# Performance work log

Measured on AMD Instinct MI355X. Metric: run time of the kernel, lower is better.

## Reference

```python
import jax, jax.numpy as jnp
import numpy as np

S_DIM, H_DIM, A_DIM, EMB, MAX_LEN = 1024, 2048, 166, 256, 20
DEC = H_DIM // 2          # decoder_hidden = 1024
VOCAB = A_DIM + 3         # 169; sos=166, eos=167, pad/ignore=168
SOS, IGNORE = A_DIM, A_DIM + 2
B = 8192


def setup_inputs() -> dict:
    key = jax.random.key(0)
    ks = jax.random.split(key, 12)
    sc = lambda fan: 1.0 / np.sqrt(fan)
    emb = jax.random.normal(ks[0], (VOCAB, EMB), jnp.float32)
    emb = emb.at[IGNORE].set(0.0)  # padding_idx=168 row is zero
    return {
        's': jax.random.normal(ks[1], (B, S_DIM), jnp.float32),
        'a_target_seq': jax.random.randint(ks[2], (B, MAX_LEN), 0, VOCAB, jnp.int32),
        'W1': jax.random.normal(ks[3], (S_DIM, H_DIM), jnp.float32) * sc(S_DIM),
        'b1': jnp.zeros((H_DIM,), jnp.float32),
        'W2': jax.random.normal(ks[4], (H_DIM, DEC), jnp.float32) * sc(H_DIM),
        'b2': jnp.zeros((DEC,), jnp.float32),
        'emb': emb,
        'Wih': jax.random.normal(ks[5], (EMB + DEC, 3 * DEC), jnp.float32) * sc(DEC),
        'Whh': jax.random.normal(ks[6], (DEC, 3 * DEC), jnp.float32) * sc(DEC),
        'bih': jnp.zeros((3 * DEC,), jnp.float32),
        'bhh': jnp.zeros((3 * DEC,), jnp.float32),
        'Wp': jax.random.normal(ks[7], (DEC, VOCAB), jnp.float32) * sc(DEC),
        'bp': jnp.zeros((VOCAB,), jnp.float32),
    }


def _gru_step(h, x, Wih, Whh, bih, bhh):
    # torch nn.GRU cell: gates ordered (r, z, n)
    gi = x @ Wih + bih                      # [B, 3H]
    gh = h @ Whh + bhh                      # [B, 3H]
    ir, iz, inn = jnp.split(gi, 3, axis=-1)
    hr, hz, hn = jnp.split(gh, 3, axis=-1)
    r = jax.nn.sigmoid(ir + hr)
    z = jax.nn.sigmoid(iz + hz)
    n = jnp.tanh(inn + r * hn)
    return (1.0 - z) * n + z * h


def reference(s, a_target_seq, W1, b1, W2, b2, emb, Wih, Whh, bih, bhh, Wp, bp):
    b = s.shape[0]
    h_s = jax.nn.relu(s @ W1 + b1) @ W2 + b2      # net(s): [B, DEC]
    h0 = h_s                                      # concatenated at every step
    # teacher forcing: input token at step t is SOS for t=0 else a_target_seq[:, t-1]
    toks = jnp.concatenate([jnp.full((b, 1), SOS, a_target_seq.dtype),
                            a_target_seq[:, :-1]], axis=1)      # [B, T]

    def step(h, tok_t):
        x = jnp.concatenate([emb[tok_t], h0], axis=-1)          # [B, EMB+DEC]
        h_new = _gru_step(h, x, Wih, Whh, bih, bhh)
        logits = h_new @ Wp + bp                                # [B, VOCAB]
        return h_new, logits

    _, logits_seq = jax.lax.scan(step, h_s, toks.T)             # [T, B, V]
    logits = jnp.transpose(logits_seq, (1, 0, 2))               # [B, T, V]

    # CrossEntropyLoss(ignore_index=IGNORE), mean over non-ignored targets
    flat_logits = logits.reshape(-1, VOCAB)
    flat_tgt = a_target_seq.reshape(-1)
    logp = jax.nn.log_softmax(flat_logits, axis=-1)
    nll = -jnp.take_along_axis(logp, flat_tgt[:, None].astype(jnp.int32), axis=-1)[:, 0]
    mask = (flat_tgt != IGNORE).astype(nll.dtype)
    loss_pred = jnp.sum(nll * mask) / jnp.maximum(jnp.sum(mask), 1.0)

    # pred_act_tsr: scatter 1.0 at per-step argmax, then drop last 3 special tokens
    eval_a = jnp.argmax(logits, axis=-1)                        # [B, T]
    pred_act_tsr = jnp.zeros((b, VOCAB), logits.dtype)
    pred_act_tsr = pred_act_tsr.at[jnp.arange(b)[:, None], eval_a].set(1.0)
    return loss_pred, pred_act_tsr[:, :-3]
```

## Files before the change

kernel.cpp:

```cpp
#include <hip/hip_runtime.h>
#include <math.h>

typedef _Float16 f16;
typedef _Float16 half8 __attribute__((ext_vector_type(8)));
typedef _Float16 half4v __attribute__((ext_vector_type(4)));
typedef float f32x4 __attribute__((ext_vector_type(4)));

#define BATCH 8192
#define SDIM  1024
#define HDIM  2048
#define DECD  1024
#define EMBD  256
#define G3    3072
#define VOCAB 169
#define VPAD  176
#define NFRAG 11
#define TLEN  20
#define SOS_TOK 166
#define IGN_TOK 168
#define OUTC  166

#define GLOAD16(gp, lp) __builtin_amdgcn_global_load_lds( \
    (const __attribute__((address_space(1))) unsigned int*)(gp), \
    (__attribute__((address_space(3))) unsigned int*)(lp), 16, 0, 0)

__device__ __forceinline__ void split2(float a, f16& h, f16& l)
{
    float hi = (fabsf(a) >= 6.103515625e-05f) ? (float)(f16)a : 0.0f;
    h = (f16)hi;
    l = (f16)((a - hi) * 2048.0f);
}

__device__ __forceinline__ float join2(f16 h, f16 l)
{
    return (float)h + (float)l * 4.8828125e-4f;
}

__device__ __forceinline__ int swz(int r, int k0)
{
    const int line = r >> 1;
    const int s = (((r & 1) << 2) | (k0 >> 3)) ^ (line & 7);
    return line * 64 + s * 8;
}

template<int MODE>
__global__ __launch_bounds__(256, 2)
void gemm16(const f16* __restrict__ Ah, const f16* __restrict__ Al,
            const f16* __restrict__ Bh, const f16* __restrict__ Bl,
            const float* __restrict__ bias, float* __restrict__ C,
            f16* __restrict__ Ch, f16* __restrict__ Cl,
            int M, int N, int K, int relu)
{
    __shared__ __align__(16) f16 lds[4][4096];

    const int nx = N >> 7;
    const int cpx = gridDim.x >> 3;
    int wg = blockIdx.x;
    wg = (wg & 7) * cpx + (wg >> 3);
    const int m0 = (wg / nx) << 7;
    const int n0 = (wg % nx) << 7;

    const int tid = threadIdx.x;
    const int w = tid >> 6;
    const int lane = tid & 63;
    const int wr = w >> 1, wc = w & 1;

    const int qq = (lane & 7) ^ (lane >> 3);
    const int row_off = ((lane >> 3) << 1) | (qq >> 2);
    const int k_off = (qq & 3) << 3;
    const f16* sb = (w == 0) ? Ah + (size_t)m0 * K
                  : (w == 1) ? Al + (size_t)m0 * K
                  : (w == 2) ? Bh + (size_t)n0 * K
                             : Bl + (size_t)n0 * K;
    sb += (size_t)row_off * K + k_off;
    f16* lb = &lds[w][0];

    int offA[4], offB[4];
    {
        const int fr = lane & 15, k0 = (lane >> 4) << 3;
#pragma unroll
        for (int t = 0; t < 4; ++t) {
            offA[t] = swz(wr * 64 + t * 16 + fr, k0);
            offB[t] = swz(wc * 64 + t * 16 + fr, k0);
        }
    }

    f32x4 acch[4][4], accl[4][4];
#pragma unroll
    for (int i = 0; i < 4; ++i)
#pragma unroll
        for (int j = 0; j < 4; ++j) { acch[i][j] = (f32x4)0.0f; accl[i][j] = (f32x4)0.0f; }

    const int nkt = K >> 5;
    const size_t K16 = (size_t)K * 16;
    for (int kt = 0; kt < nkt; ++kt) {
        const f16* s = sb + kt * 32;
#pragma unroll
        for (int i = 0; i < 8; ++i)
            GLOAD16(s + (size_t)i * K16, lb + i * 512);
        __syncthreads();

        half8 fah[4], fbh[4], fal[4], fbl[4];
#pragma unroll
        for (int t = 0; t < 4; ++t) {
            fah[t] = *(const half8*)&lds[0][offA[t]];
            fal[t] = *(const half8*)&lds[1][offA[t]];
            fbh[t] = *(const half8*)&lds[2][offB[t]];
            fbl[t] = *(const half8*)&lds[3][offB[t]];
        }
#pragma unroll
        for (int i = 0; i < 4; ++i)
#pragma unroll
            for (int j = 0; j < 4; ++j) {
                acch[i][j] = __builtin_amdgcn_mfma_f32_16x16x32_f16(fah[i], fbh[j], acch[i][j], 0, 0, 0);
                accl[i][j] = __builtin_amdgcn_mfma_f32_16x16x32_f16(fal[i], fbh[j], accl[i][j], 0, 0, 0);
                accl[i][j] = __builtin_amdgcn_mfma_f32_16x16x32_f16(fah[i], fbl[j], accl[i][j], 0, 0, 0);
            }
        __syncthreads();
    }

    const float inv2048 = 4.8828125e-4f;
    const int fr = lane & 15;
    const int fq = lane >> 4;
#pragma unroll
    for (int j = 0; j < 4; ++j) {
        const int col = n0 + wc * 64 + j * 16 + fr;
        const float bc = bias[col];
#pragma unroll
        for (int i = 0; i < 4; ++i) {
            const int row0 = m0 + wr * 64 + i * 16 + fq * 4;
            const f32x4 vh = acch[i][j], vl = accl[i][j];
#pragma unroll
            for (int r = 0; r < 4; ++r) {
                float v = vh[r] + vl[r] * inv2048 + bc;
                if (relu) v = fmaxf(v, 0.0f);
                const size_t o = (size_t)(row0 + r) * N + col;
                if constexpr (MODE & 1) C[o] = v;
                if constexpr (MODE & 2) { f16 hh, hl; split2(v, hh, hl); Ch[o] = hh; Cl[o] = hl; }
            }
        }
    }
}

#define STAGE(SET, KT) do {                                                        \
    const int ko_ = (KT) * 32 + k_off;                                             \
    if (w == 0) {                                                                  \
        const f16* sp = hch + (size_t)(m0 + row_off) * DECD + ko_;                 \
        _Pragma("unroll") for (int i_ = 0; i_ < 8; ++i_)                           \
            GLOAD16(sp + (size_t)i_ * (16 * DECD), &lds[SET][i_ * 512]);           \
    } else if (w == 1) {                                                           \
        const f16* sp = hcl + (size_t)(m0 + row_off) * DECD + ko_;                 \
        _Pragma("unroll") for (int i_ = 0; i_ < 8; ++i_)                           \
            GLOAD16(sp + (size_t)i_ * (16 * DECD), &lds[SET][4096 + i_ * 512]);    \
    } else if (w == 2) {                                                           \
        _Pragma("unroll") for (int g_ = 0; g_ < 3; ++g_) {                         \
            const f16* sp = whh + (size_t)(g_ * DECD + n0 + row_off) * DECD + ko_; \
            _Pragma("unroll") for (int i_ = 0; i_ < 4; ++i_)                       \
                GLOAD16(sp + (size_t)i_ * (16 * DECD),                             \
                        &lds[SET][8192 + g_ * 4096 + i_ * 512]);                   \
        }                                                                          \
    } else {                                                                       \
        _Pragma("unroll") for (int g_ = 0; g_ < 3; ++g_) {                         \
            const f16* sp = whl + (size_t)(g_ * DECD + n0 + row_off) * DECD + ko_; \
            _Pragma("unroll") for (int i_ = 0; i_ < 4; ++i_)                       \
                GLOAD16(sp + (size_t)i_ * (16 * DECD),                             \
                        &lds[SET][8192 + g_ * 4096 + 2048 + i_ * 512]);            \
        }                                                                          \
    }                                                                              \
} while (0)

__global__ __launch_bounds__(256, 1)
void gru_fused(const f16* __restrict__ hch, const f16* __restrict__ hcl,
               const f16* __restrict__ whh, const f16* __restrict__ whl,
               const float* __restrict__ bhh, const float* __restrict__ gx0,
               const float* __restrict__ tg, const int* __restrict__ tseq,
               int t, f16* __restrict__ hnh, f16* __restrict__ hnl)
{
    __shared__ __align__(16) f16 lds[2][20480];

    const int cpx = gridDim.x >> 3;
    int wg = blockIdx.x;
    wg = (wg & 7) * cpx + (wg >> 3);
    const int m0 = (wg >> 4) << 7;
    const int n0 = (wg & 15) << 6;

    const int tid = threadIdx.x, w = tid >> 6, lane = tid & 63;
    const int wr = w >> 1, wc = w & 1;

    const int qq = (lane & 7) ^ (lane >> 3);
    const int row_off = ((lane >> 3) << 1) | (qq >> 2);
    const int k_off = (qq & 3) << 3;

    const int fr = lane & 15, kq8 = (lane >> 4) << 3;
    int offA[4], offB[2];
#pragma unroll
    for (int i = 0; i < 4; ++i) offA[i] = swz(wr * 64 + i * 16 + fr, kq8);
#pragma unroll
    for (int j = 0; j < 2; ++j) offB[j] = swz(wc * 32 + j * 16 + fr, kq8);

    f32x4 aH[3][4][2], aL[3][4][2];
#pragma unroll
    for (int g = 0; g < 3; ++g)
#pragma unroll
        for (int i = 0; i < 4; ++i)
#pragma unroll
            for (int j = 0; j < 2; ++j) { aH[g][i][j] = (f32x4)0.0f; aL[g][i][j] = (f32x4)0.0f; }

    STAGE(0, 0);
    __syncthreads();

#pragma unroll 2
    for (int kt = 0; kt < DECD / 32; ++kt) {
        const int cur = kt & 1;
        if (kt < DECD / 32 - 1) STAGE(cur ^ 1, kt + 1);

        half8 fah[4], fal[4];
#pragma unroll
        for (int i = 0; i < 4; ++i) {
            fah[i] = *(const half8*)&lds[cur][offA[i]];
            fal[i] = *(const half8*)&lds[cur][4096 + offA[i]];
        }
#pragma unroll
        for (int g = 0; g < 3; ++g) {
            half8 bh[2], bl[2];
#pragma unroll
            for (int j = 0; j < 2; ++j) {
                bh[j] = *(const half8*)&lds[cur][8192 + g * 4096 + offB[j]];
                bl[j] = *(const half8*)&lds[cur][8192 + g * 4096 + 2048 + offB[j]];
            }
#pragma unroll
            for (int i = 0; i < 4; ++i)
#pragma unroll
                for (int j = 0; j < 2; ++j) {
                    aH[g][i][j] = __builtin_amdgcn_mfma_f32_16x16x32_f16(fah[i], bh[j], aH[g][i][j], 0, 0, 0);
                    aL[g][i][j] = __builtin_amdgcn_mfma_f32_16x16x32_f16(fal[i], bh[j], aL[g][i][j], 0, 0, 0);
                    aL[g][i][j] = __builtin_amdgcn_mfma_f32_16x16x32_f16(fah[i], bl[j], aL[g][i][j], 0, 0, 0);
                }
        }
        __syncthreads();
    }

    const float inv = 4.8828125e-4f;
    const int fq = lane >> 4;
    float br[2], bz[2], bn[2];
#pragma unroll
    for (int j = 0; j < 2; ++j) {
        const int col = n0 + wc * 32 + j * 16 + fr;
        br[j] = bhh[col];
        bz[j] = bhh[DECD + col];
        bn[j] = bhh[2 * DECD + col];
    }
#pragma unroll
    for (int i = 0; i < 4; ++i) {
#pragma unroll
        for (int r = 0; r < 4; ++r) {
            const int row = m0 + wr * 64 + i * 16 + fq * 4 + r;
            const int tok = (t == 0) ? SOS_TOK : tseq[(size_t)row * TLEN + (t - 1)];
            const size_t gb = (size_t)row * G3;
            const size_t tb = (size_t)tok * G3;
#pragma unroll
            for (int j = 0; j < 2; ++j) {
                const int col = n0 + wc * 32 + j * 16 + fr;
                const float ghr = aH[0][i][j][r] + aL[0][i][j][r] * inv + br[j];
                const float ghz = aH[1][i][j][r] + aL[1][i][j][r] * inv + bz[j];
                const float ghn = aH[2][i][j][r] + aL[2][i][j][r] * inv + bn[j];
                const float gir = gx0[gb + col] + tg[tb + col];
                const float giz = gx0[gb + DECD + col] + tg[tb + DECD + col];
                const float gin = gx0[gb + 2 * DECD + col] + tg[tb + 2 * DECD + col];
                const float rr = 1.f / (1.f + expf(-(gir + ghr)));
                const float zz = 1.f / (1.f + expf(-(giz + ghz)));
                const float nn = tanhf(gin + rr * ghn);
                const size_t hidx = (size_t)row * DECD + col;
                const float hp = join2(hch[hidx], hcl[hidx]);
                const float hv = (1.f - zz) * nn + zz * hp;
                f16 a_, b_; split2(hv, a_, b_);
                hnh[hidx] = a_;
                hnl[hidx] = b_;
            }
        }
    }
}

__global__ __launch_bounds__(256)
void transpose_split(const float* __restrict__ Wm, f16* __restrict__ th, f16* __restrict__ tl,
                     int K, int N)
{
    __shared__ float tile[32][33];
    const int n0 = blockIdx.x << 5, k0 = blockIdx.y << 5;
    const int tx = threadIdx.x & 31, ty = threadIdx.x >> 5;
#pragma unroll
    for (int j = 0; j < 32; j += 8)
        tile[ty + j][tx] = Wm[(size_t)(k0 + ty + j) * N + n0 + tx];
    __syncthreads();
#pragma unroll
    for (int j = 0; j < 32; j += 8) {
        const float a = tile[tx][ty + j];
        f16 hh, hl; split2(a, hh, hl);
        const size_t o = (size_t)(n0 + ty + j) * K + k0 + tx;
        th[o] = hh; tl[o] = hl;
    }
}

__global__ __launch_bounds__(256)
void wp_split(const float* __restrict__ Wp, f16* __restrict__ wph, f16* __restrict__ wpl)
{
    const int k = blockIdx.x * 256 + threadIdx.x;
    const int n = blockIdx.y;
    const float a = (n < VOCAB) ? Wp[(size_t)k * VOCAB + n] : 0.0f;
    f16 h, l; split2(a, h, l);
    wph[(size_t)n * DECD + k] = h;
    wpl[(size_t)n * DECD + k] = l;
}

__global__ __launch_bounds__(256)
void split_act(const float* __restrict__ x, f16* __restrict__ xh, f16* __restrict__ xl)
{
    const int i = blockIdx.x * 256 + threadIdx.x;
    const float4 v = ((const float4*)x)[i];
    half4v hh, hl;
#pragma unroll
    for (int c = 0; c < 4; ++c) { f16 a, b; split2((&v.x)[c], a, b); hh[c] = a; hl[c] = b; }
    ((half4v*)xh)[i] = hh;
    ((half4v*)xl)[i] = hl;
}

__global__ __launch_bounds__(256)
void tok_gi(const float* __restrict__ emb, const float* __restrict__ Wih,
            float* __restrict__ tg)
{
    __shared__ float es[EMBD];
    const int v = blockIdx.y;
    const int n = blockIdx.x * 256 + threadIdx.x;
    es[threadIdx.x] = emb[(size_t)v * EMBD + threadIdx.x];
    __syncthreads();
    float s = 0.f;
#pragma unroll 8
    for (int k = 0; k < EMBD; ++k)
        s = fmaf(es[k], Wih[(size_t)k * G3 + n], s);
    tg[(size_t)v * G3 + n] = s;
}

__global__ __launch_bounds__(256)
void logits_mfma(const f16* __restrict__ hh, const f16* __restrict__ hl,
                 const f16* __restrict__ wph, const f16* __restrict__ wpl,
                 const float* __restrict__ bp, const int* __restrict__ tseq,
                 int t, float* __restrict__ pred, float* __restrict__ accb)
{
    __shared__ float red[3][64][44];
    const int tid = threadIdx.x, wv = tid >> 6, lane = tid & 63;
    const int b0 = blockIdx.x << 4;
    const int fr = lane & 15, kq = lane >> 4;
    const int kb = wv << 8;

    const f16* pa_h = hh + (size_t)(b0 + fr) * DECD + kb + kq * 8;
    const f16* pa_l = hl + (size_t)(b0 + fr) * DECD + kb + kq * 8;
    const f16* pb_h = wph + (size_t)fr * DECD + kb + kq * 8;
    const f16* pb_l = wpl + (size_t)fr * DECD + kb + kq * 8;

    f32x4 acch[NFRAG], accl[NFRAG];
#pragma unroll
    for (int f = 0; f < NFRAG; ++f) { acch[f] = (f32x4)0.0f; accl[f] = (f32x4)0.0f; }

#pragma unroll 2
    for (int kt = 0; kt < 8; ++kt) {
        const int ko = kt * 32;
        const half8 a_h = *(const half8*)(pa_h + ko);
        const half8 a_l = *(const half8*)(pa_l + ko);
#pragma unroll
        for (int f = 0; f < NFRAG; ++f) {
            const half8 b_h = *(const half8*)(pb_h + (size_t)f * 16 * DECD + ko);
            const half8 b_l = *(const half8*)(pb_l + (size_t)f * 16 * DECD + ko);
            acch[f] = __builtin_amdgcn_mfma_f32_16x16x32_f16(a_h, b_h, acch[f], 0, 0, 0);
            accl[f] = __builtin_amdgcn_mfma_f32_16x16x32_f16(a_l, b_h, accl[f], 0, 0, 0);
            accl[f] = __builtin_amdgcn_mfma_f32_16x16x32_f16(a_h, b_l, accl[f], 0, 0, 0);
        }
    }

    float v[44];
#pragma unroll
    for (int f = 0; f < NFRAG; ++f)
#pragma unroll
        for (int r = 0; r < 4; ++r)
            v[f * 4 + r] = acch[f][r] + accl[f][r] * 4.8828125e-4f;

    if (wv > 0) {
#pragma unroll
        for (int idx = 0; idx < 44; ++idx) red[wv - 1][lane][idx] = v[idx];
    }
    __syncthreads();
    if (wv != 0) return;

#pragma unroll
    for (int ww = 0; ww < 3; ++ww)
#pragma unroll
        for (int idx = 0; idx < 44; ++idx) v[idx] += red[ww][lane][idx];

    float wnll = 0.f, wcnt = 0.f;
#pragma unroll
    for (int r = 0; r < 4; ++r) {
        const int b = b0 + kq * 4 + r;
        float vv[NFRAG];
        float m = -3.0e38f; int mi = 0;
#pragma unroll
        for (int f = 0; f < NFRAG; ++f) {
            const int col = f * 16 + fr;
            const float bb = (col < VOCAB) ? bp[col] : -1.0e30f;
            vv[f] = v[f * 4 + r] + bb;
            if (vv[f] > m) { m = vv[f]; mi = col; }
        }
#pragma unroll
        for (int off = 8; off >= 1; off >>= 1) {
            const float om = __shfl_xor(m, off);
            const int   oi = __shfl_xor(mi, off);
            if (om > m || (om == m && oi < mi)) { m = om; mi = oi; }
        }
        const int tgt = tseq[(size_t)b * TLEN + t];
        float se = 0.f, tl = 0.f;
#pragma unroll
        for (int f = 0; f < NFRAG; ++f) {
            se += expf(vv[f] - m);
            if ((tgt >> 4) == f && (tgt & 15) == fr) tl = vv[f];
        }
#pragma unroll
        for (int off = 8; off >= 1; off >>= 1) {
            se += __shfl_xor(se, off);
            tl += __shfl_xor(tl, off);
        }
        if (fr == 0) {
            if (mi < OUTC) pred[(size_t)b * OUTC + mi] = 1.0f;
            if (tgt != IGN_TOK) { wnll += m + logf(se) - tl; wcnt += 1.f; }
        }
    }
    wnll += __shfl_xor(wnll, 16); wnll += __shfl_xor(wnll, 32);
    wcnt += __shfl_xor(wcnt, 16); wcnt += __shfl_xor(wcnt, 32);
    if (lane == 0) {
        atomicAdd(&accb[0], wnll);
        atomicAdd(&accb[1], wcnt);
    }
}

__global__ void finalize_loss(const float* __restrict__ accb, float* __restrict__ out)
{
    out[0] = accb[0] / fmaxf(accb[1], 1.f);
}

extern "C" void kernel_launch(void* const* d_in, const int* in_sizes, int n_in,
                              void* d_out, int out_size, void* d_ws, size_t ws_size,
                              hipStream_t stream)
{
    const float* s    = (const float*)d_in[0];
    const int*   aseq = (const int*)  d_in[1];
    const float* W1   = (const float*)d_in[2];
    const float* b1   = (const float*)d_in[3];
    const float* W2   = (const float*)d_in[4];
    const float* b2   = (const float*)d_in[5];
    const float* emb  = (const float*)d_in[6];
    const float* Wih  = (const float*)d_in[7];
    const float* Whh  = (const float*)d_in[8];
    const float* bih  = (const float*)d_in[9];
    const float* bhh  = (const float*)d_in[10];
    const float* Wp   = (const float*)d_in[11];
    const float* bp   = (const float*)d_in[12];
    float* outp = (float*)d_out;
    char* W = (char*)d_ws;

    const size_t SZ_H = (size_t)BATCH * DECD * 2;
    const size_t o_gx0 = 0;
    const size_t o_hAh = o_gx0 + (size_t)BATCH * G3 * 4;
    const size_t o_hAl = o_hAh + SZ_H;
    const size_t o_hBh = o_hAl + SZ_H;
    const size_t o_hBl = o_hBh + SZ_H;
    const size_t o_tg  = o_hBl + SZ_H;
    const size_t o_whh = o_tg  + (size_t)VOCAB * G3 * 4;
    const size_t o_whl = o_whh + (size_t)DECD * G3 * 2;
    const size_t o_wph = o_whl + (size_t)DECD * G3 * 2;
    const size_t o_wpl = o_wph + (size_t)VPAD * DECD * 2;
    const size_t o_acc = o_wpl + (size_t)VPAD * DECD * 2;
    const size_t need  = o_acc + 256;
    if (ws_size < need) return;

    float* gx0  = (float*)(W + o_gx0);
    f16*   hAh  = (f16*)(W + o_hAh);
    f16*   hAl  = (f16*)(W + o_hAl);
    f16*   hBh  = (f16*)(W + o_hBh);
    f16*   hBl  = (f16*)(W + o_hBl);
    float* tg   = (float*)(W + o_tg);
    f16*   whh  = (f16*)(W + o_whh);
    f16*   whl  = (f16*)(W + o_whl);
    f16*   wph  = (f16*)(W + o_wph);
    f16*   wpl  = (f16*)(W + o_wpl);
    float* accb = (float*)(W + o_acc);

    f16* h1h = (f16*)(W + o_gx0);
    f16* h1l = (f16*)(W + o_gx0 + (size_t)BATCH * HDIM * 2);
    f16* w1h = (f16*)(W + o_gx0 + (size_t)BATCH * HDIM * 4);
    f16* w1l = (f16*)(W + o_gx0 + (size_t)BATCH * HDIM * 4 + (size_t)SDIM * HDIM * 2);
    f16* w2h = w1h;
    f16* w2l = (f16*)(W + o_gx0 + (size_t)BATCH * HDIM * 4 + (size_t)HDIM * DECD * 2);
    f16* sh  = (f16*)(W + o_hBh);
    f16* sl  = (f16*)(W + o_hBh + (size_t)BATCH * SDIM * 2);
    f16* wih = whh;
    f16* wil = whl;

    hipMemsetAsync(d_out, 0, (size_t)out_size * sizeof(float), stream);
    hipMemsetAsync(accb, 0, 2 * sizeof(float), stream);

    split_act<<<dim3(BATCH * SDIM / 4 / 256), 256, 0, stream>>>(s, sh, sl);
    transpose_split<<<dim3(HDIM/32, SDIM/32), 256, 0, stream>>>(W1, w1h, w1l, SDIM, HDIM);
    tok_gi<<<dim3(G3/256, VOCAB), 256, 0, stream>>>(emb, Wih, tg);
    wp_split<<<dim3(DECD/256, VPAD), 256, 0, stream>>>(Wp, wph, wpl);

    gemm16<2><<<dim3((BATCH/128)*(HDIM/128)), 256, 0, stream>>>(
        sh, sl, w1h, w1l, b1, nullptr, h1h, h1l, BATCH, HDIM, SDIM, 1);

    transpose_split<<<dim3(DECD/32, HDIM/32), 256, 0, stream>>>(W2, w2h, w2l, HDIM, DECD);
    gemm16<2><<<dim3((BATCH/128)*(DECD/128)), 256, 0, stream>>>(
        h1h, h1l, w2h, w2l, b2, nullptr, hAh, hAl, BATCH, DECD, HDIM, 0);

    transpose_split<<<dim3(G3/32, DECD/32), 256, 0, stream>>>(Wih + (size_t)EMBD * G3, wih, wil, DECD, G3);
    gemm16<1><<<dim3((BATCH/128)*(G3/128)), 256, 0, stream>>>(
        hAh, hAl, wih, wil, bih, gx0, nullptr, nullptr, BATCH, G3, DECD, 0);

    transpose_split<<<dim3(G3/32, DECD/32), 256, 0, stream>>>(Whh, whh, whl, DECD, G3);

    f16 *ch = hAh, *cl = hAl, *nh = hBh, *nl = hBl;
    for (int t = 0; t < TLEN; ++t) {
        gru_fused<<<dim3((BATCH/128)*(DECD/64)), 256, 0, stream>>>(
            ch, cl, whh, whl, bhh, gx0, tg, aseq, t, nh, nl);
        logits_mfma<<<dim3(BATCH/16), 256, 0, stream>>>(
            nh, nl, wph, wpl, bp, aseq, t, outp + 1, accb);
        f16* tmp;
        tmp = ch; ch = nh; nh = tmp;
        tmp = cl; cl = nl; nl = tmp;
    }
    finalize_loss<<<1, 1, 0, stream>>>(accb, outp);
}
```

Before: 7.115 ms.

## Shrink GRU tile to 128x32 and drop LDS double buffering for occupancy

The recurrent GRU kernel now computes a 128x32 output tile per gate instead of 128x64. This halves the accumulator registers and doubles the grid size. LDS use drops to a single buffer of about 28KB, and launch bounds now allow 3 blocks per CU, so several workgroups can overlap to hide latency. In exchange, the prefetch double buffering is removed, adding a sync after each stage, and each A tile is reloaded by twice as many blocks, which raises global and L2 traffic per unit of MFMA work.

```diff
diff --git a/kernel.cpp b/kernel.cpp
--- a/kernel.cpp
+++ b/kernel.cpp
@@ -142,47 +142,47 @@
     }
 }
 
-#define STAGE(SET, KT) do {                                                        \
+#define STAGE_V2(KT) do {                                                          \
     const int ko_ = (KT) * 32 + k_off;                                             \
     if (w == 0) {                                                                  \
         const f16* sp = hch + (size_t)(m0 + row_off) * DECD + ko_;                 \
         _Pragma("unroll") for (int i_ = 0; i_ < 8; ++i_)                           \
-            GLOAD16(sp + (size_t)i_ * (16 * DECD), &lds[SET][i_ * 512]);           \
+            GLOAD16(sp + (size_t)i_ * (16 * DECD), &lds[i_ * 512]);                \
     } else if (w == 1) {                                                           \
         const f16* sp = hcl + (size_t)(m0 + row_off) * DECD + ko_;                 \
         _Pragma("unroll") for (int i_ = 0; i_ < 8; ++i_)                           \
-            GLOAD16(sp + (size_t)i_ * (16 * DECD), &lds[SET][4096 + i_ * 512]);    \
+            GLOAD16(sp + (size_t)i_ * (16 * DECD), &lds[4096 + i_ * 512]);         \
     } else if (w == 2) {                                                           \
         _Pragma("unroll") for (int g_ = 0; g_ < 3; ++g_) {                         \
             const f16* sp = whh + (size_t)(g_ * DECD + n0 + row_off) * DECD + ko_; \
-            _Pragma("unroll") for (int i_ = 0; i_ < 4; ++i_)                       \
+            _Pragma("unroll") for (int i_ = 0; i_ < 2; ++i_)                       \
                 GLOAD16(sp + (size_t)i_ * (16 * DECD),                             \
-                        &lds[SET][8192 + g_ * 4096 + i_ * 512]);                   \
+                        &lds[8192 + g_ * 1024 + i_ * 512]);                        \
         }                                                                          \
     } else {                                                                       \
         _Pragma("unroll") for (int g_ = 0; g_ < 3; ++g_) {                         \
             const f16* sp = whl + (size_t)(g_ * DECD + n0 + row_off) * DECD + ko_; \
-            _Pragma("unroll") for (int i_ = 0; i_ < 4; ++i_)                       \
+            _Pragma("unroll") for (int i_ = 0; i_ < 2; ++i_)                       \
                 GLOAD16(sp + (size_t)i_ * (16 * DECD),                             \
-                        &lds[SET][8192 + g_ * 4096 + 2048 + i_ * 512]);            \
+                        &lds[11264 + g_ * 1024 + i_ * 512]);                       \
         }                                                                          \
     }                                                                              \
 } while (0)
 
-__global__ __launch_bounds__(256, 1)
+__global__ __launch_bounds__(256, 3)
 void gru_fused(const f16* __restrict__ hch, const f16* __restrict__ hcl,
                const f16* __restrict__ whh, const f16* __restrict__ whl,
                const float* __restrict__ bhh, const float* __restrict__ gx0,
                const float* __restrict__ tg, const int* __restrict__ tseq,
                int t, f16* __restrict__ hnh, f16* __restrict__ hnl)
 {
-    __shared__ __align__(16) f16 lds[2][20480];
+    __shared__ __align__(16) f16 lds[14336];
 
     const int cpx = gridDim.x >> 3;
     int wg = blockIdx.x;
     wg = (wg & 7) * cpx + (wg >> 3);
-    const int m0 = (wg >> 4) << 7;
-    const int n0 = (wg & 15) << 6;
+    const int m0 = (wg >> 5) << 7;
+    const int n0 = (wg & 31) << 5;
 
     const int tid = threadIdx.x, w = tid >> 6, lane = tid & 63;
     const int wr = w >> 1, wc = w & 1;
@@ -192,64 +192,47 @@
     const int k_off = (qq & 3) << 3;
 
     const int fr = lane & 15, kq8 = (lane >> 4) << 3;
-    int offA[4], offB[2];
+    int offA[4];
 #pragma unroll
     for (int i = 0; i < 4; ++i) offA[i] = swz(wr * 64 + i * 16 + fr, kq8);
-#pragma unroll
-    for (int j = 0; j < 2; ++j) offB[j] = swz(wc * 32 + j * 16 + fr, kq8);
-
-    f32x4 aH[3][4][2], aL[3][4][2];
+    const int offB = swz(wc * 16 + fr, kq8);
+
+    f32x4 aH[3][4], aL[3][4];
 #pragma unroll
     for (int g = 0; g < 3; ++g)
 #pragma unroll
-        for (int i = 0; i < 4; ++i)
-#pragma unroll
-            for (int j = 0; j < 2; ++j) { aH[g][i][j] = (f32x4)0.0f; aL[g][i][j] = (f32x4)0.0f; }
-
-    STAGE(0, 0);
-    __syncthreads();
-
-#pragma unroll 2
+        for (int i = 0; i < 4; ++i) { aH[g][i] = (f32x4)0.0f; aL[g][i] = (f32x4)0.0f; }
+
     for (int kt = 0; kt < DECD / 32; ++kt) {
-        const int cur = kt & 1;
-        if (kt < DECD / 32 - 1) STAGE(cur ^ 1, kt + 1);
+        STAGE_V2(kt);
+        __syncthreads();
 
         half8 fah[4], fal[4];
 #pragma unroll
         for (int i = 0; i < 4; ++i) {
-            fah[i] = *(const half8*)&lds[cur][offA[i]];
-            fal[i] = *(const half8*)&lds[cur][4096 + offA[i]];
+            fah[i] = *(const half8*)&lds[offA[i]];
+            fal[i] = *(const half8*)&lds[4096 + offA[i]];
         }
 #pragma unroll
         for (int g = 0; g < 3; ++g) {
-            half8 bh[2], bl[2];
-#pragma unroll
-            for (int j = 0; j < 2; ++j) {
-                bh[j] = *(const half8*)&lds[cur][8192 + g * 4096 + offB[j]];
-                bl[j] = *(const half8*)&lds[cur][8192 + g * 4096 + 2048 + offB[j]];
+            const half8 bh = *(const half8*)&lds[8192 + g * 1024 + offB];
+            const half8 bl = *(const half8*)&lds[11264 + g * 1024 + offB];
+#pragma unroll
+            for (int i = 0; i < 4; ++i) {
+                aH[g][i] = __builtin_amdgcn_mfma_f32_16x16x32_f16(fah[i], bh, aH[g][i], 0, 0, 0);
+                aL[g][i] = __builtin_amdgcn_mfma_f32_16x16x32_f16(fal[i], bh, aL[g][i], 0, 0, 0);
+                aL[g][i] = __builtin_amdgcn_mfma_f32_16x16x32_f16(fah[i], bl, aL[g][i], 0, 0, 0);
             }
-#pragma unroll
-            for (int i = 0; i < 4; ++i)
-#pragma unroll
-                for (int j = 0; j < 2; ++j) {
-                    aH[g][i][j] = __builtin_amdgcn_mfma_f32_16x16x32_f16(fah[i], bh[j], aH[g][i][j], 0, 0, 0);
-                    aL[g][i][j] = __builtin_amdgcn_mfma_f32_16x16x32_f16(fal[i], bh[j], aL[g][i][j], 0, 0, 0);
-                    aL[g][i][j] = __builtin_amdgcn_mfma_f32_16x16x32_f16(fah[i], bl[j], aL[g][i][j], 0, 0, 0);
-                }
         }
         __syncthreads();
     }
 
     const float inv = 4.8828125e-4f;
     const int fq = lane >> 4;
-    float br[2], bz[2], bn[2];
-#pragma unroll
-    for (int j = 0; j < 2; ++j) {
-        const int col = n0 + wc * 32 + j * 16 + fr;
-        br[j] = bhh[col];
-        bz[j] = bhh[DECD + col];
-        bn[j] = bhh[2 * DECD + col];
-    }
+    const int col = n0 + wc * 16 + fr;
+    const float br = bhh[col];
+    const float bz = bhh[DECD + col];
+    const float bn = bhh[2 * DECD + col];
 #pragma unroll
     for (int i = 0; i < 4; ++i) {
 #pragma unroll
@@ -258,25 +241,21 @@
             const int tok = (t == 0) ? SOS_TOK : tseq[(size_t)row * TLEN + (t - 1)];
             const size_t gb = (size_t)row * G3;
             const size_t tb = (size_t)tok * G3;
-#pragma unroll
-            for (int j = 0; j < 2; ++j) {
-                const int col = n0 + wc * 32 + j * 16 + fr;
-                const float ghr = aH[0][i][j][r] + aL[0][i][j][r] * inv + br[j];
-                const float ghz = aH[1][i][j][r] + aL[1][i][j][r] * inv + bz[j];
-                const float ghn = aH[2][i][j][r] + aL[2][i][j][r] * inv + bn[j];
-                const float gir = gx0[gb + col] + tg[tb + col];
-                const float giz = gx0[gb + DECD + col] + tg[tb + DECD + col];
-                const float gin = gx0[gb + 2 * DECD + col] + tg[tb + 2 * DECD + col];
-                const float rr = 1.f / (1.f + expf(-(gir + ghr)));
-                const float zz = 1.f / (1.f + expf(-(giz + ghz)));
-                const float nn = tanhf(gin + rr * ghn);
-                const size_t hidx = (size_t)row * DECD + col;
-                const float hp = join2(hch[hidx], hcl[hidx]);
-                const float hv = (1.f - zz) * nn + zz * hp;
-                f16 a_, b_; split2(hv, a_, b_);
-                hnh[hidx] = a_;
-                hnl[hidx] = b_;
-            }
+            const float ghr = aH[0][i][r] + aL[0][i][r] * inv + br;
+            const float ghz = aH[1][i][r] + aL[1][i][r] * inv + bz;
+            const float ghn = aH[2][i][r] + aL[2][i][r] * inv + bn;
+            const float gir = gx0[gb + col] + tg[tb + col];
+            const float giz = gx0[gb + DECD + col] + tg[tb + DECD + col];
+            const float gin = gx0[gb + 2 * DECD + col] + tg[tb + 2 * DECD + col];
+            const float rr = 1.f / (1.f + expf(-(gir + ghr)));
+            const float zz = 1.f / (1.f + expf(-(giz + ghz)));
+            const float nn = tanhf(gin + rr * ghn);
+            const size_t hidx = (size_t)row * DECD + col;
+            const float hp = join2(hch[hidx], hcl[hidx]);
+            const float hv = (1.f - zz) * nn + zz * hp;
+            f16 a_, b_; split2(hv, a_, b_);
+            hnh[hidx] = a_;
+            hnl[hidx] = b_;
         }
     }
 }
@@ -525,7 +504,7 @@
 
     f16 *ch = hAh, *cl = hAl, *nh = hBh, *nl = hBl;
     for (int t = 0; t < TLEN; ++t) {
-        gru_fused<<<dim3((BATCH/128)*(DECD/64)), 256, 0, stream>>>(
+        gru_fused<<<dim3((BATCH/128)*(DECD/32)), 256, 0, stream>>>(
             ch, cl, whh, whl, bhh, gx0, tg, aseq, t, nh, nl);
         logits_mfma<<<dim3(BATCH/16), 256, 0, stream>>>(
             nh, nl, wph, wpl, bp, aseq, t, outp + 1, accb);
```

Result: faster. 5.952 ms (-16.3%).
